# Performance work log

Measured on AMD Instinct MI355X. Metric: run time of the kernel, lower is better.

Reference implementation:

```python
import jax, jax.numpy as jnp
import numpy as np
from jax.scipy.special import logsumexp

B, N_LC, N_TE, D = 4, 2048, 2048, 256
ITERS = 100  # Sinkhorn iterations


def _mlp2(x, W1, b1, W2, b2):
    # 2-layer MLP with ReLU (DETR-style MLP, num_layers=2)
    h = jax.nn.relu(x @ W1.T + b1)
    return h @ W2.T + b2


def _log_optimal_transport(scores, alpha, iters):
    b, m, n = scores.shape
    ms = jnp.float32(m)
    ns = jnp.float32(n)
    # augment score matrix with dustbin row/col -> [b, m+1, n+1]
    bins0 = jnp.broadcast_to(alpha, (b, m, 1))
    bins1 = jnp.broadcast_to(alpha, (b, 1, n))
    binsc = jnp.broadcast_to(alpha, (b, 1, 1))
    Z = jnp.concatenate([
        jnp.concatenate([scores, bins0], axis=-1),
        jnp.concatenate([bins1, binsc], axis=-1)], axis=1)
    norm = -jnp.log(ms + ns)
    log_mu = jnp.concatenate([jnp.full((m,), norm), jnp.log(ns)[None] + norm])
    log_nu = jnp.concatenate([jnp.full((n,), norm), jnp.log(ms)[None] + norm])
    log_mu = jnp.broadcast_to(log_mu[None], (b, m + 1))
    log_nu = jnp.broadcast_to(log_nu[None], (b, n + 1))

    def step(carry, _):
        u, v = carry
        u = log_mu - logsumexp(Z + v[:, None, :], axis=2)
        v = log_nu - logsumexp(Z + u[:, :, None], axis=1)
        return (u, v), None

    u0 = jnp.zeros_like(log_mu)
    v0 = jnp.zeros_like(log_nu)
    (u, v), _ = jax.lax.scan(step, (u0, v0), None, length=iters)
    return Z + u[:, :, None] + v[:, None, :] - norm


def setup_inputs() -> dict:
    key = jax.random.key(0)
    ks = jax.random.split(key, 8)
    s = 1.0 / np.sqrt(D).astype(np.float32)
    return {
        "quer_feat_lc": jax.random.normal(ks[0], (B, N_LC, D), jnp.float32),
        "quer_feat_te": jax.random.normal(ks[1], (B, N_TE, D), jnp.float32),
        "W1_lc": jax.random.normal(ks[2], (D, D), jnp.float32) * s,
        "b1_lc": jnp.zeros((D,), jnp.float32),
        "W2_lc": jax.random.normal(ks[3], (D, D), jnp.float32) * s,
        "b2_lc": jnp.zeros((D,), jnp.float32),
        "W1_te": jax.random.normal(ks[4], (D, D), jnp.float32) * s,
        "b1_te": jnp.zeros((D,), jnp.float32),
        "W2_te": jax.random.normal(ks[5], (D, D), jnp.float32) * s,
        "b2_te": jnp.zeros((D,), jnp.float32),
        "bin_score": jnp.ones((), jnp.float32),
    }


def reference(quer_feat_lc, quer_feat_te, W1_lc, b1_lc, W2_lc, b2_lc,
              W1_te, b1_te, W2_te, b2_te, bin_score):
    f1 = _mlp2(quer_feat_lc, W1_lc, b1_lc, W2_lc, b2_lc)  # [B, N_LC, D]
    f2 = _mlp2(quer_feat_te, W1_te, b1_te, W2_te, b2_te)  # [B, N_TE, D]
    scores = jnp.einsum('bnc,bmc->bnm', f1, f2) / jnp.sqrt(jnp.float32(D))
    Z = _log_optimal_transport(scores, bin_score, ITERS)  # [B, N_LC+1, N_TE+1]
    return jnp.exp(Z)
```

## Files before the change

kernel.cpp:

```cpp
#include <hip/hip_runtime.h>
#include <hip/hip_fp16.h>

#define NQ   2048
#define NB   4
#define DD   256
#define M1   2049
#define STR  2064
#define SINK_ITERS 100
#define PNWG 256
#define PTPB 1024

typedef __attribute__((ext_vector_type(8))) short short8;
typedef __attribute__((ext_vector_type(4))) float floatx4;
typedef __attribute__((ext_vector_type(2))) float floatx2;
typedef _Float16 h2 __attribute__((ext_vector_type(2)));

__device__ __forceinline__ unsigned short f2bf(float f) {
  unsigned u = __float_as_uint(f);
  u += 0x7FFF + ((u >> 16) & 1);
  return (unsigned short)(u >> 16);
}

__device__ __forceinline__ unsigned char f2fp8(float f) {
  unsigned short u = __half_as_ushort(__float2half(f));
  return (unsigned char)((u + 0x7F + ((u >> 8) & 1)) >> 8);
}

__device__ __forceinline__ h2 as_h2(unsigned x) {
  union { unsigned u; h2 h; } c; c.u = x; return c.h;
}

__global__ void k_cvt6(const float* __restrict__ x_lc, const float* __restrict__ x_te,
                       const float* __restrict__ w1lc, const float* __restrict__ w2lc,
                       const float* __restrict__ w1te, const float* __restrict__ w2te,
                       unsigned short* __restrict__ Xlc, unsigned short* __restrict__ Xte,
                       unsigned short* __restrict__ Wb) {
  const int NX4 = (NB * NQ * DD) / 4;
  const int NW4 = (DD * DD) / 4;
  int i4 = blockIdx.x * blockDim.x + threadIdx.x;
  const float* src; unsigned short* dst; int off;
  if (i4 < NX4)            { src = x_lc; dst = Xlc; off = i4; }
  else if (i4 < 2 * NX4)   { src = x_te; dst = Xte; off = i4 - NX4; }
  else {
    int k = i4 - 2 * NX4;
    int seg = k / NW4;
    off = k - seg * NW4;
    src = (seg == 0) ? w1lc : (seg == 1) ? w2lc : (seg == 2) ? w1te : w2te;
    dst = Wb + seg * 65536;
  }
  float4 f = ((const float4*)src)[off];
  ushort4 o;
  o.x = f2bf(f.x); o.y = f2bf(f.y); o.z = f2bf(f.z); o.w = f2bf(f.w);
  ((ushort4*)dst)[off] = o;
}

template<int MODE>
__global__ __launch_bounds__(256, 2)
void k_gemm_bt(const unsigned short* __restrict__ A,
               const unsigned short* __restrict__ Bt,
               void* __restrict__ Out, void* __restrict__ Out8,
               const float* __restrict__ bias, const float* __restrict__ bias2,
               int K, long aBatch, long bBatch, long oBatch, int ostride)
{
  __shared__ __align__(16) unsigned short lA[128 * 32];
  __shared__ __align__(16) unsigned short lB[128 * 32];
  const int tid  = threadIdx.x;
  const int lane = tid & 63;
  const int w    = tid >> 6;
  const int wm   = (w >> 1) * 64;
  const int wn   = (w & 1) * 64;
  const long bz  = blockIdx.z;
  const unsigned short* Ab = A  + bz * aBatch + (long)blockIdx.y * 128 * K;
  const unsigned short* Bb = Bt + bz * bBatch + (long)blockIdx.x * 128 * K;
  const float* bp = (bz == 0) ? bias : bias2;

  floatx4 acc[4][4];
  #pragma unroll
  for (int i = 0; i < 4; i++)
    #pragma unroll
    for (int j = 0; j < 4; j++) acc[i][j] = (floatx4){0.f, 0.f, 0.f, 0.f};

  for (int kt = 0; kt < K; kt += 32) {
    __syncthreads();
    #pragma unroll
    for (int s0 = 0; s0 < 512; s0 += 256) {
      int s = s0 + tid;
      int row = s >> 2, part = s & 3;
      ((uint4*)lA)[s] = *(const uint4*)(Ab + (long)row * K + kt + part * 8);
      ((uint4*)lB)[s] = *(const uint4*)(Bb + (long)row * K + kt + part * 8);
    }
    __syncthreads();
    const int kq = (lane >> 4) * 8;
    const int rl = lane & 15;
    short8 af[4], bf[4];
    #pragma unroll
    for (int t = 0; t < 4; t++) {
      af[t] = *(const short8*)(lA + (wm + t * 16 + rl) * 32 + kq);
      bf[t] = *(const short8*)(lB + (wn + t * 16 + rl) * 32 + kq);
    }
    #pragma unroll
    for (int i = 0; i < 4; i++)
      #pragma unroll
      for (int j = 0; j < 4; j++)
        acc[i][j] = __builtin_amdgcn_mfma_f32_16x16x32_bf16(af[i], bf[j], acc[i][j], 0, 0, 0);
  }

  const int cl = lane & 15, qd = lane >> 4;
  #pragma unroll
  for (int i = 0; i < 4; i++)
    #pragma unroll
    for (int j = 0; j < 4; j++) {
      const int col = blockIdx.x * 128 + wn + j * 16 + cl;
      const float bcol = (MODE >= 2) ? 0.f : bp[col];
      #pragma unroll
      for (int r = 0; r < 4; r++) {
        const long row = (long)blockIdx.y * 128 + wm + i * 16 + qd * 4 + r;
        float v = acc[i][j][r];
        if (MODE == 0) {
          v += bcol; v = v > 0.f ? v : 0.f;
          ((unsigned short*)Out)[bz * oBatch + row * ostride + col] = f2bf(v);
        } else if (MODE == 1) {
          v += bcol;
          ((unsigned short*)Out)[bz * oBatch + row * ostride + col] = f2bf(v);
        } else {
          v *= 0.0625f;
          v = fminf(fmaxf(v, -15.f), 10.9f);
          float e = __expf(v);
          const long idx = bz * oBatch + row * ostride + col;
          if (MODE == 2) ((__half*)Out)[idx] = __float2half(e);
          ((unsigned char*)Out8)[idx] = f2fp8(e);
        }
      }
    }
}

__global__ void k_fillinit(__half* __restrict__ E, const float* __restrict__ alphaPtr,
                           float* __restrict__ ev, unsigned* __restrict__ bar) {
  const float ea = __expf(*alphaPtr);
  const int idx = blockIdx.x * blockDim.x + threadIdx.x;
  const int n1 = NB * NQ * 16;
  if (idx < n1) {
    int b = idx / (NQ * 16);
    int rr = idx - b * NQ * 16;
    int i = rr >> 4;
    int j = 2048 + (rr & 15);
    E[((long)b * M1 + i) * STR + j] = (j == 2048) ? __float2half(ea) : __float2half(0.f);
  } else {
    int k = idx - n1;
    if (k < NB * STR) {
      int b = k / STR;
      int j = k - b * STR;
      E[((long)b * M1 + 2048) * STR + j] = (j <= 2048) ? __float2half(ea) : __float2half(0.f);
    }
  }
  if (idx < NB * STR) ev[idx] = 1.0f;
  if (idx < 2048) bar[idx] = 0u;
}

__device__ __forceinline__ void st_agent(float* p, float v) {
  __hip_atomic_store(p, v, __ATOMIC_RELAXED, __HIP_MEMORY_SCOPE_AGENT);
}
__device__ __forceinline__ float ld_agent(const float* p) {
  return __hip_atomic_load(p, __ATOMIC_RELAXED, __HIP_MEMORY_SCOPE_AGENT);
}
__device__ __forceinline__ unsigned long long ld64_agent(const unsigned long long* p) {
  return __hip_atomic_load(p, __ATOMIC_RELAXED, __HIP_MEMORY_SCOPE_AGENT);
}
__device__ __forceinline__ unsigned ld_u32_agent(const unsigned* p) {
  return __hip_atomic_load(p, __ATOMIC_RELAXED, __HIP_MEMORY_SCOPE_AGENT);
}

__device__ __forceinline__ float wave_sum(float s) {
  #pragma unroll
  for (int o = 32; o; o >>= 1) s += __shfl_xor(s, o);
  return s;
}

__device__ __forceinline__ float dot16e5(uint4 hv, const unsigned* wp, float s) {
  const unsigned* u = (const unsigned*)&hv;
#if __has_builtin(__builtin_amdgcn_fdot2) && __has_builtin(__builtin_amdgcn_perm)
  #pragma unroll
  for (int q = 0; q < 4; q++) {
    unsigned lo = __builtin_amdgcn_perm(u[q], 0u, 0x05000400u);
    unsigned hi = __builtin_amdgcn_perm(u[q], 0u, 0x07000600u);
    s = __builtin_amdgcn_fdot2(as_h2(lo), as_h2(wp[2 * q]),     s, false);
    s = __builtin_amdgcn_fdot2(as_h2(hi), as_h2(wp[2 * q + 1]), s, false);
  }
#else
  const unsigned char* p = (const unsigned char*)&hv;
  #pragma unroll
  for (int t = 0; t < 16; t++) {
    unsigned short he = (unsigned short)p[t] << 8;
    unsigned wdw = wp[t >> 1];
    unsigned short hw = (t & 1) ? (unsigned short)(wdw >> 16) : (unsigned short)(wdw & 0xFFFF);
    s += __half2float(*reinterpret_cast<__half*>(&he)) *
         __half2float(*reinterpret_cast<__half*>(&hw));
  }
#endif
  return s;
}

__global__ __launch_bounds__(PTPB, 4)
void k_sink(const unsigned char* __restrict__ E8, const unsigned char* __restrict__ ET8,
            float* __restrict__ eu, float* __restrict__ ev,
            const float* __restrict__ alphaPtr, unsigned* __restrict__ bar)
{
  __shared__ __align__(16) unsigned char rows[131072];
  __shared__ __align__(16) unsigned svh[1160];
  __shared__ float sdust;
  const int tid  = threadIdx.x;
  const int wg   = blockIdx.x;
  const int b    = wg >> 6;
  const int g    = wg & 63;
  const int wv   = tid >> 6;
  const int lane = tid & 63;
  const int r0   = (g * 16 + wv) * 2;
  const float ea = __expf(alphaPtr[0]);
  const unsigned char* E8r  = E8  + ((long)b * M1 + r0) * STR;
  const unsigned char* ET8r = ET8 + ((long)b * M1 + r0) * STR;
  float* ub = eu + b * STR;
  float* vb = ev + b * STR;
  unsigned* cnt = bar + b * 64;
  unsigned* gen = bar + b * 64 + 32;
  const bool dustwave = (g == 63) && (wv == 15);
  const int sslot = (tid >> 9) * 576 + (tid & 511) + ((tid & 511) >> 3);

  {
    uint4* dw = (uint4*)(rows + wv * 8192);
    dw[lane]       = *(const uint4*)(E8r  +        lane * 16);
    dw[64 + lane]  = *(const uint4*)(E8r  + 1024 + lane * 16);
    dw[128 + lane] = *(const uint4*)(E8r  + STR  +        lane * 16);
    dw[192 + lane] = *(const uint4*)(E8r  + STR  + 1024 + lane * 16);
    dw[256 + lane] = *(const uint4*)(ET8r +        lane * 16);
    dw[320 + lane] = *(const uint4*)(ET8r + 1024 + lane * 16);
    dw[384 + lane] = *(const uint4*)(ET8r + STR  +        lane * 16);
    dw[448 + lane] = *(const uint4*)(ET8r + STR  + 1024 + lane * 16);
  }

  const unsigned* w0 = svh + 9 * lane;
  const unsigned* w1 = svh + 576 + 9 * lane;
  const unsigned ONES2 = 0x3C003C00u;

  unsigned phase = 0;
  for (int it = 0; it < 2 * SINK_ITERS; ++it) {
    const float* vin = (it & 1) ? ub : vb;
    float*      vout = (it & 1) ? vb : ub;

    {
      unsigned long long w8 = ld64_agent((const unsigned long long*)(vin + 2 * tid));
      float flo = __uint_as_float((unsigned)w8) * 4096.f;
      float fhi = __uint_as_float((unsigned)(w8 >> 32)) * 4096.f;
      unsigned pk = ((unsigned)__half_as_ushort(__float2half(fhi)) << 16)
                  |  (unsigned)__half_as_ushort(__float2half(flo));
      svh[sslot] = pk;
      if (tid == 0) sdust = ld_agent(vin + 2048) * 4096.f;
    }
    __syncthreads();

    const unsigned char* Rl = rows + wv * 8192 + ((it & 1) << 12);
    uint4 h0c0 = *(const uint4*)(Rl +        lane * 16);
    uint4 h0c1 = *(const uint4*)(Rl + 1024 + lane * 16);
    uint4 h1c0 = *(const uint4*)(Rl + 2048 + lane * 16);
    uint4 h1c1 = *(const uint4*)(Rl + 3072 + lane * 16);
    float a0 = dot16e5(h0c1, w1, dot16e5(h0c0, w0, 0.f));
    float a1 = dot16e5(h1c1, w1, dot16e5(h1c0, w0, 0.f));
    a0 = wave_sum(a0);
    a1 = wave_sum(a1);
    if (lane == 0) {
      const float wd = ea * sdust;
      st_agent(vout + r0,     1.f / (a0 + wd));
      st_agent(vout + r0 + 1, 1.f / (a1 + wd));
    }

    if (dustwave) {
      float s = 0.f;
#if __has_builtin(__builtin_amdgcn_fdot2)
      #pragma unroll
      for (int k = 0; k < 8; k++) s = __builtin_amdgcn_fdot2(as_h2(w0[k]), as_h2(ONES2), s, false);
      #pragma unroll
      for (int k = 0; k < 8; k++) s = __builtin_amdgcn_fdot2(as_h2(w1[k]), as_h2(ONES2), s, false);
#else
      #pragma unroll
      for (int k = 0; k < 8; k++) {
        unsigned a = w0[k], c = w1[k];
        unsigned short x0 = (unsigned short)a, x1 = (unsigned short)(a >> 16);
        unsigned short y0 = (unsigned short)c, y1 = (unsigned short)(c >> 16);
        s += __half2float(*reinterpret_cast<__half*>(&x0)) + __half2float(*reinterpret_cast<__half*>(&x1))
           + __half2float(*reinterpret_cast<__half*>(&y0)) + __half2float(*reinterpret_cast<__half*>(&y1));
      }
#endif
      s = wave_sum(s);
      if (lane == 0) st_agent(vout + 2048, 2048.f / (ea * (s + sdust)));
    }

    ++phase;
    __syncthreads();
    if (tid == 0) {
      unsigned gpre = ld_u32_agent(gen);
      unsigned old = __hip_atomic_fetch_add(cnt, 1u, __ATOMIC_RELAXED, __HIP_MEMORY_SCOPE_AGENT);
      if (old == phase * 64u - 1u) {
        __hip_atomic_store(gen, phase, __ATOMIC_RELAXED, __HIP_MEMORY_SCOPE_AGENT);
      } else {
        while (gpre < phase) {
          __builtin_amdgcn_s_sleep(1);
          gpre = ld_u32_agent(gen);
        }
      }
    }
    __syncthreads();
  }
}

__global__ void k_final(const __half* __restrict__ E, const float* __restrict__ eu,
                        const float* __restrict__ ev, float* __restrict__ out) {
  const int wv = blockIdx.x;
  const int b = wv / M1;
  const int i = wv - b * M1;
  const __half* R = E + ((long)b * M1 + i) * STR;
  const float ui = eu[b * STR + i] * 4096.f;
  const float* evb = ev + b * STR;
  float* orow = out + ((long)b * M1 + i) * M1;
  for (int j = threadIdx.x; j < M1; j += blockDim.x)
    orow[j] = __half2float(R[j]) * ui * evb[j];
}

extern "C" void kernel_launch(void* const* d_in, const int* in_sizes, int n_in,
                              void* d_out, int out_size, void* d_ws, size_t ws_size,
                              hipStream_t stream) {
  const float* x_lc  = (const float*)d_in[0];
  const float* x_te  = (const float*)d_in[1];
  const float* W1_lc = (const float*)d_in[2];
  const float* b1_lc = (const float*)d_in[3];
  const float* W2_lc = (const float*)d_in[4];
  const float* b2_lc = (const float*)d_in[5];
  const float* W1_te = (const float*)d_in[6];
  const float* b1_te = (const float*)d_in[7];
  const float* W2_te = (const float*)d_in[8];
  const float* b2_te = (const float*)d_in[9];
  const float* alpha = (const float*)d_in[10];

  char* ws = (char*)d_ws;
  unsigned short* Xlc = (unsigned short*)(ws + 0);
  unsigned short* Wb  = (unsigned short*)(ws + 8388608);
  unsigned short* H   = (unsigned short*)(ws + 8912896);
  unsigned short* F   = (unsigned short*)(ws + 0);
  __half* E  = (__half*)(ws + 21495808);
  unsigned char* E8  = (unsigned char*)(ws + 55328896);
  unsigned char* ET8 = (unsigned char*)(ws + 72245440);
  float* eu  = (float*)(ws + 89161984);
  float* ev  = (float*)(ws + 89195008);
  unsigned* bar = (unsigned*)(ws + 89228032);

  unsigned short* Xte = Xlc + 2097152;

  k_cvt6<<<4352, 256, 0, stream>>>(x_lc, x_te, W1_lc, W2_lc, W1_te, W2_te,
                                   Xlc, Xte, Wb);

  k_gemm_bt<0><<<dim3(2, 64, 2), 256, 0, stream>>>(Xlc, Wb,         H, nullptr, b1_lc, b1_te,
                                                   DD, 2097152, 131072, 2097152, DD);
  k_gemm_bt<1><<<dim3(2, 64, 2), 256, 0, stream>>>(H,   Wb + 65536, F, nullptr, b2_lc, b2_te,
                                                   DD, 2097152, 131072, 2097152, DD);

  unsigned short* F1 = F;
  unsigned short* F2 = F + 2097152;
  const long ab = (long)NQ * DD;
  const long ob = (long)M1 * STR;
  k_gemm_bt<2><<<dim3(16, 16, NB), 256, 0, stream>>>(F1, F2, E,  E8,  nullptr, nullptr, DD, ab, ab, ob, STR);
  k_gemm_bt<3><<<dim3(16, 16, NB), 256, 0, stream>>>(F2, F1, nullptr, ET8, nullptr, nullptr, DD, ab, ab, ob, STR);

  const int nfill = NB * NQ * 16 + NB * STR;
  k_fillinit<<<(nfill + 255) / 256, 256, 0, stream>>>(E, alpha, ev, bar);

  k_sink<<<PNWG, PTPB, 0, stream>>>(E8, ET8, eu, ev, alpha, bar);

  k_final<<<NB * M1, 256, 0, stream>>>(E, eu, ev, (float*)d_out);
}
```

Baseline: 789.0 us.

## Fuse transpose GEMM into score GEMM, merge fill into prep, pack u/v as fp16

The separate transposed score GEMM is removed. The main score GEMM now writes the transposed fp8 copy directly as packed 4-byte column stores. The fill/init kernel is folded into the conversion kernel, which saves a launch. Sinkhorn u/v vectors are stored pre-scaled as packed fp16 pairs, so each iteration loads one 32-bit word per thread and skips the float-to-half conversion. The transposed stores are strided and may be poorly coalesced, and keeping u/v in fp16 storage may cost some precision.

Result: no change. 799.1 us (+1.3%).

```diff
diff --git a/kernel.cpp b/kernel.cpp
--- a/kernel.cpp
+++ b/kernel.cpp
@@ -6,13 +6,13 @@
 #define DD   256
 #define M1   2049
 #define STR  2064
+#define UVS  1088
 #define SINK_ITERS 100
 #define PNWG 256
 #define PTPB 1024
 
 typedef __attribute__((ext_vector_type(8))) short short8;
 typedef __attribute__((ext_vector_type(4))) float floatx4;
-typedef __attribute__((ext_vector_type(2))) float floatx2;
 typedef _Float16 h2 __attribute__((ext_vector_type(2)));
 
 __device__ __forceinline__ unsigned short f2bf(float f) {
@@ -30,35 +30,69 @@
   union { unsigned u; h2 h; } c; c.u = x; return c.h;
 }
 
-__global__ void k_cvt6(const float* __restrict__ x_lc, const float* __restrict__ x_te,
+__global__ void k_prep(const float* __restrict__ x_lc, const float* __restrict__ x_te,
                        const float* __restrict__ w1lc, const float* __restrict__ w2lc,
                        const float* __restrict__ w1te, const float* __restrict__ w2te,
                        unsigned short* __restrict__ Xlc, unsigned short* __restrict__ Xte,
-                       unsigned short* __restrict__ Wb) {
+                       unsigned short* __restrict__ Wb, __half* __restrict__ E,
+                       const float* __restrict__ alphaPtr, unsigned* __restrict__ ev,
+                       unsigned* __restrict__ bar) {
   const int NX4 = (NB * NQ * DD) / 4;
   const int NW4 = (DD * DD) / 4;
-  int i4 = blockIdx.x * blockDim.x + threadIdx.x;
-  const float* src; unsigned short* dst; int off;
-  if (i4 < NX4)            { src = x_lc; dst = Xlc; off = i4; }
-  else if (i4 < 2 * NX4)   { src = x_te; dst = Xte; off = i4 - NX4; }
-  else {
-    int k = i4 - 2 * NX4;
-    int seg = k / NW4;
-    off = k - seg * NW4;
-    src = (seg == 0) ? w1lc : (seg == 1) ? w2lc : (seg == 2) ? w1te : w2te;
-    dst = Wb + seg * 65536;
-  }
-  float4 f = ((const float4*)src)[off];
-  ushort4 o;
-  o.x = f2bf(f.x); o.y = f2bf(f.y); o.z = f2bf(f.z); o.w = f2bf(f.w);
-  ((ushort4*)dst)[off] = o;
+  const int bx = blockIdx.x;
+  if (bx < 4352) {
+    int i4 = bx * 256 + threadIdx.x;
+    const float* src; unsigned short* dst; int off;
+    if (i4 < NX4)            { src = x_lc; dst = Xlc; off = i4; }
+    else if (i4 < 2 * NX4)   { src = x_te; dst = Xte; off = i4 - NX4; }
+    else {
+      int k = i4 - 2 * NX4;
+      int seg = k / NW4;
+      off = k - seg * NW4;
+      src = (seg == 0) ? w1lc : (seg == 1) ? w2lc : (seg == 2) ? w1te : w2te;
+      dst = Wb + seg * 65536;
+    }
+    float4 f = ((const float4*)src)[off];
+    ushort4 o;
+    o.x = f2bf(f.x); o.y = f2bf(f.y); o.z = f2bf(f.z); o.w = f2bf(f.w);
+    ((ushort4*)dst)[off] = o;
+    return;
+  }
+  const int idx = (bx - 4352) * 256 + threadIdx.x;
+  const float ea = __expf(*alphaPtr);
+  const int n1 = NB * NQ * 16;
+  if (idx < n1) {
+    int b = idx / (NQ * 16);
+    int rr = idx - b * NQ * 16;
+    int i = rr >> 4;
+    int j = 2048 + (rr & 15);
+    E[((long)b * M1 + i) * STR + j] = (j == 2048) ? __float2half(ea) : __float2half(0.f);
+    return;
+  }
+  int k = idx - n1;
+  if (k < NB * STR) {
+    int b = k / STR;
+    int j = k - b * STR;
+    E[((long)b * M1 + 2048) * STR + j] = (j <= 2048) ? __float2half(ea) : __float2half(0.f);
+    return;
+  }
+  int m = k - NB * STR;
+  if (m < NB * UVS) {
+    int bloc = m / UVS;
+    int slot = m - bloc * UVS;
+    ev[m] = (slot < 1024) ? 0x6C006C00u
+          : (slot == 1024 ? __float_as_uint(4096.f) : 0u);
+    return;
+  }
+  int q = m - NB * UVS;
+  if (q < 2048) bar[q] = 0u;
 }
 
 template<int MODE>
 __global__ __launch_bounds__(256, 2)
 void k_gemm_bt(const unsigned short* __restrict__ A,
                const unsigned short* __restrict__ Bt,
-               void* __restrict__ Out, void* __restrict__ Out8,
+               void* __restrict__ Out, void* __restrict__ Out8, void* __restrict__ OutT8,
                const float* __restrict__ bias, const float* __restrict__ bias2,
                int K, long aBatch, long bBatch, long oBatch, int ostride)
 {
@@ -112,9 +146,11 @@
     for (int j = 0; j < 4; j++) {
       const int col = blockIdx.x * 128 + wn + j * 16 + cl;
       const float bcol = (MODE >= 2) ? 0.f : bp[col];
+      const long rowbase = (long)blockIdx.y * 128 + wm + i * 16 + qd * 4;
+      unsigned pk = 0;
       #pragma unroll
       for (int r = 0; r < 4; r++) {
-        const long row = (long)blockIdx.y * 128 + wm + i * 16 + qd * 4 + r;
+        const long row = rowbase + r;
         float v = acc[i][j][r];
         if (MODE == 0) {
           v += bcol; v = v > 0.f ? v : 0.f;
@@ -127,44 +163,20 @@
           v = fminf(fmaxf(v, -15.f), 10.9f);
           float e = __expf(v);
           const long idx = bz * oBatch + row * ostride + col;
-          if (MODE == 2) ((__half*)Out)[idx] = __float2half(e);
-          ((unsigned char*)Out8)[idx] = f2fp8(e);
+          ((__half*)Out)[idx] = __float2half(e);
+          unsigned char f8 = f2fp8(e);
+          ((unsigned char*)Out8)[idx] = f8;
+          pk |= (unsigned)f8 << (8 * r);
         }
       }
-    }
-}
-
-__global__ void k_fillinit(__half* __restrict__ E, const float* __restrict__ alphaPtr,
-                           float* __restrict__ ev, unsigned* __restrict__ bar) {
-  const float ea = __expf(*alphaPtr);
-  const int idx = blockIdx.x * blockDim.x + threadIdx.x;
-  const int n1 = NB * NQ * 16;
-  if (idx < n1) {
-    int b = idx / (NQ * 16);
-    int rr = idx - b * NQ * 16;
-    int i = rr >> 4;
-    int j = 2048 + (rr & 15);
-    E[((long)b * M1 + i) * STR + j] = (j == 2048) ? __float2half(ea) : __float2half(0.f);
-  } else {
-    int k = idx - n1;
-    if (k < NB * STR) {
-      int b = k / STR;
-      int j = k - b * STR;
-      E[((long)b * M1 + 2048) * STR + j] = (j <= 2048) ? __float2half(ea) : __float2half(0.f);
-    }
-  }
-  if (idx < NB * STR) ev[idx] = 1.0f;
-  if (idx < 2048) bar[idx] = 0u;
-}
-
-__device__ __forceinline__ void st_agent(float* p, float v) {
+      if (MODE == 2) {
+        *(unsigned*)((unsigned char*)OutT8 + bz * oBatch + (long)col * ostride + rowbase) = pk;
+      }
+    }
+}
+
+__device__ __forceinline__ void st_u32_agent(unsigned* p, unsigned v) {
   __hip_atomic_store(p, v, __ATOMIC_RELAXED, __HIP_MEMORY_SCOPE_AGENT);
-}
-__device__ __forceinline__ float ld_agent(const float* p) {
-  return __hip_atomic_load(p, __ATOMIC_RELAXED, __HIP_MEMORY_SCOPE_AGENT);
-}
-__device__ __forceinline__ unsigned long long ld64_agent(const unsigned long long* p) {
-  return __hip_atomic_load(p, __ATOMIC_RELAXED, __HIP_MEMORY_SCOPE_AGENT);
 }
 __device__ __forceinline__ unsigned ld_u32_agent(const unsigned* p) {
   return __hip_atomic_load(p, __ATOMIC_RELAXED, __HIP_MEMORY_SCOPE_AGENT);
@@ -202,7 +214,7 @@
 
 __global__ __launch_bounds__(PTPB, 4)
 void k_sink(const unsigned char* __restrict__ E8, const unsigned char* __restrict__ ET8,
-            float* __restrict__ eu, float* __restrict__ ev,
+            unsigned* __restrict__ eu, unsigned* __restrict__ ev,
             const float* __restrict__ alphaPtr, unsigned* __restrict__ bar)
 {
   __shared__ __align__(16) unsigned char rows[131072];
@@ -218,8 +230,8 @@
   const float ea = __expf(alphaPtr[0]);
   const unsigned char* E8r  = E8  + ((long)b * M1 + r0) * STR;
   const unsigned char* ET8r = ET8 + ((long)b * M1 + r0) * STR;
-  float* ub = eu + b * STR;
-  float* vb = ev + b * STR;
+  unsigned* ub = eu + b * UVS;
+  unsigned* vb = ev + b * UVS;
   unsigned* cnt = bar + b * 64;
   unsigned* gen = bar + b * 64 + 32;
   const bool dustwave = (g == 63) && (wv == 15);
@@ -243,17 +255,13 @@
 
   unsigned phase = 0;
   for (int it = 0; it < 2 * SINK_ITERS; ++it) {
-    const float* vin = (it & 1) ? ub : vb;
-    float*      vout = (it & 1) ? vb : ub;
+    const unsigned* vin = (it & 1) ? ub : vb;
+    unsigned*      vout = (it & 1) ? vb : ub;
 
     {
-      unsigned long long w8 = ld64_agent((const unsigned long long*)(vin + 2 * tid));
-      float flo = __uint_as_float((unsigned)w8) * 4096.f;
-      float fhi = __uint_as_float((unsigned)(w8 >> 32)) * 4096.f;
-      unsigned pk = ((unsigned)__half_as_ushort(__float2half(fhi)) << 16)
-                  |  (unsigned)__half_as_ushort(__float2half(flo));
-      svh[sslot] = pk;
-      if (tid == 0) sdust = ld_agent(vin + 2048) * 4096.f;
+      unsigned pkv = ld_u32_agent(vin + tid);
+      svh[sslot] = pkv;
+      if (tid == 0) sdust = __uint_as_float(ld_u32_agent(vin + 1024));
     }
     __syncthreads();
 
@@ -268,8 +276,11 @@
     a1 = wave_sum(a1);
     if (lane == 0) {
       const float wd = ea * sdust;
-      st_agent(vout + r0,     1.f / (a0 + wd));
-      st_agent(vout + r0 + 1, 1.f / (a1 + wd));
+      float u0 = 4096.f / (a0 + wd);
+      float u1 = 4096.f / (a1 + wd);
+      unsigned pk = ((unsigned)__half_as_ushort(__float2half(u1)) << 16)
+                  |  (unsigned)__half_as_ushort(__float2half(u0));
+      st_u32_agent(vout + (r0 >> 1), pk);
     }
 
     if (dustwave) {
@@ -290,7 +301,8 @@
       }
 #endif
       s = wave_sum(s);
-      if (lane == 0) st_agent(vout + 2048, 2048.f / (ea * (s + sdust)));
+      if (lane == 0)
+        st_u32_agent(vout + 1024, __float_as_uint(8388608.f / (ea * (s + sdust))));
     }
 
     ++phase;
@@ -311,17 +323,35 @@
   }
 }
 
-__global__ void k_final(const __half* __restrict__ E, const float* __restrict__ eu,
-                        const float* __restrict__ ev, float* __restrict__ out) {
-  const int wv = blockIdx.x;
-  const int b = wv / M1;
-  const int i = wv - b * M1;
+__global__ void k_final(const __half* __restrict__ E, const unsigned* __restrict__ eu,
+                        const unsigned* __restrict__ ev, float* __restrict__ out) {
+  const int wvb = blockIdx.x;
+  const int b = wvb / M1;
+  const int i = wvb - b * M1;
   const __half* R = E + ((long)b * M1 + i) * STR;
-  const float ui = eu[b * STR + i] * 4096.f;
-  const float* evb = ev + b * STR;
+  const unsigned* ub = eu + b * UVS;
+  const unsigned* vb = ev + b * UVS;
+  float ui;
+  if (i < 2048) {
+    unsigned d = ub[i >> 1];
+    unsigned short h = (i & 1) ? (unsigned short)(d >> 16) : (unsigned short)(d & 0xFFFF);
+    ui = __half2float(*reinterpret_cast<const __half*>(&h));
+  } else {
+    ui = __uint_as_float(ub[1024]);
+  }
+  ui *= (1.f / 4096.f);
   float* orow = out + ((long)b * M1 + i) * M1;
-  for (int j = threadIdx.x; j < M1; j += blockDim.x)
-    orow[j] = __half2float(R[j]) * ui * evb[j];
+  for (int j = threadIdx.x; j < M1; j += blockDim.x) {
+    float vj;
+    if (j < 2048) {
+      unsigned d = vb[j >> 1];
+      unsigned short h = (j & 1) ? (unsigned short)(d >> 16) : (unsigned short)(d & 0xFFFF);
+      vj = __half2float(*reinterpret_cast<const __half*>(&h));
+    } else {
+      vj = __uint_as_float(vb[1024]);
+    }
+    orow[j] = __half2float(R[j]) * ui * vj;
+  }
 }
 
 extern "C" void kernel_launch(void* const* d_in, const int* in_sizes, int n_in,
@@ -347,29 +377,26 @@
   __half* E  = (__half*)(ws + 21495808);
   unsigned char* E8  = (unsigned char*)(ws + 55328896);
   unsigned char* ET8 = (unsigned char*)(ws + 72245440);
-  float* eu  = (float*)(ws + 89161984);
-  float* ev  = (float*)(ws + 89195008);
+  unsigned* eu  = (unsigned*)(ws + 89161984);
+  unsigned* ev  = (unsigned*)(ws + 89195008);
   unsigned* bar = (unsigned*)(ws + 89228032);
 
   unsigned short* Xte = Xlc + 2097152;
 
-  k_cvt6<<<4352, 256, 0, stream>>>(x_lc, x_te, W1_lc, W2_lc, W1_te, W2_te,
-                                   Xlc, Xte, Wb);
-
-  k_gemm_bt<0><<<dim3(2, 64, 2), 256, 0, stream>>>(Xlc, Wb,         H, nullptr, b1_lc, b1_te,
-                                                   DD, 2097152, 131072, 2097152, DD);
-  k_gemm_bt<1><<<dim3(2, 64, 2), 256, 0, stream>>>(H,   Wb + 65536, F, nullptr, b2_lc, b2_te,
-                                                   DD, 2097152, 131072, 2097152, DD);
+  k_prep<<<4352 + 570, 256, 0, stream>>>(x_lc, x_te, W1_lc, W2_lc, W1_te, W2_te,
+                                         Xlc, Xte, Wb, E, alpha, ev, bar);
+
+  k_gemm_bt<0><<<dim3(2, 64, 2), 256, 0, stream>>>(Xlc, Wb,         H, nullptr, nullptr,
+                                                   b1_lc, b1_te, DD, 2097152, 131072, 2097152, DD);
+  k_gemm_bt<1><<<dim3(2, 64, 2), 256, 0, stream>>>(H,   Wb + 65536, F, nullptr, nullptr,
+                                                   b2_lc, b2_te, DD, 2097152, 131072, 2097152, DD);
 
   unsigned short* F1 = F;
   unsigned short* F2 = F + 2097152;
   const long ab = (long)NQ * DD;
   const long ob = (long)M1 * STR;
-  k_gemm_bt<2><<<dim3(16, 16, NB), 256, 0, stream>>>(F1, F2, E,  E8,  nullptr, nullptr, DD, ab, ab, ob, STR);
-  k_gemm_bt<3><<<dim3(16, 16, NB), 256, 0, stream>>>(F2, F1, nullptr, ET8, nullptr, nullptr, DD, ab, ab, ob, STR);
-
-  const int nfill = NB * NQ * 16 + NB * STR;
-  k_fillinit<<<(nfill + 255) / 256, 256, 0, stream>>>(E, alpha, ev, bar);
+  k_gemm_bt<2><<<dim3(16, 16, NB), 256, 0, stream>>>(F1, F2, E, E8, ET8,
+                                                     nullptr, nullptr, DD, ab, ab, ob, STR);
 
   k_sink<<<PNWG, PTPB, 0, stream>>>(E8, ET8, eu, ev, alpha, bar);
 
```
